# Optimization experiments

Hardware: AMD Instinct MI355X
Metric: run time of the kernel (lower is better)

Reference implementation:

```python
import jax, jax.numpy as jnp
import numpy as np

EPS = 1e-12  # matches tf.math.l2_normalize epsilon used by K.l2_normalize


def setup_inputs() -> dict:
    key = jax.random.key(0)
    k1, k2, k3 = jax.random.split(key, 3)
    B, N, C = 512, 256, 256
    x = jax.random.normal(k1, (B, N, C), dtype=jnp.float32)
    kernel = jax.random.normal(k2, (N, 1), dtype=jnp.float32)
    bias = jax.random.normal(k3, (N,), dtype=jnp.float32)
    return {"x": x, "kernel": kernel, "bias": bias}


def reference(x, kernel, bias):
    # x: [B, N, C]; kernel: [N, 1]; bias: [N]
    N = x.shape[-2]
    mid = N // 2
    # self-similarity: [B, N, N]
    sim = jnp.einsum('bnc,bmc->bnm', x, x)
    # l2-normalize along last axis (tf semantics: x * rsqrt(max(sum(x^2), eps)))
    coe = sim * jax.lax.rsqrt(jnp.maximum(jnp.sum(sim * sim, axis=-1, keepdims=True), EPS))
    # center row scaled by kernel: [B, N, 1]
    coe0 = coe[:, mid, :][..., None] * kernel
    # gating logits: [B, N, 1]
    w = jnp.einsum('bnm,bmk->bnk', coe, coe0) + bias[None, :, None]
    # softmax over spatial axis N, broadcast-multiply with input
    return jax.nn.softmax(w, axis=-2) * x
```

## Files before the change

### kernel.cpp

```cpp
#include <hip/hip_runtime.h>

#define B_N 256
#define B_C 256
#define MID 128
#define NELEM (B_N * B_C)

typedef float f32x4 __attribute__((ext_vector_type(4)));
typedef __bf16 bf16x8 __attribute__((ext_vector_type(8)));
typedef short short8 __attribute__((ext_vector_type(8)));

__device__ __forceinline__ float bf2f(unsigned short h) {
  return __builtin_bit_cast(float, (unsigned int)h << 16);
}

__device__ __forceinline__ short8 cvt8(float4 a, float4 b) {
  union { unsigned short us[8]; short8 v; } P;
  P.us[0] = __builtin_bit_cast(unsigned short, (__bf16)a.x);
  P.us[1] = __builtin_bit_cast(unsigned short, (__bf16)a.y);
  P.us[2] = __builtin_bit_cast(unsigned short, (__bf16)a.z);
  P.us[3] = __builtin_bit_cast(unsigned short, (__bf16)a.w);
  P.us[4] = __builtin_bit_cast(unsigned short, (__bf16)b.x);
  P.us[5] = __builtin_bit_cast(unsigned short, (__bf16)b.y);
  P.us[6] = __builtin_bit_cast(unsigned short, (__bf16)b.z);
  P.us[7] = __builtin_bit_cast(unsigned short, (__bf16)b.w);
  return P.v;
}

__global__ __launch_bounds__(512, 1) void spat_attn(
    const float* __restrict__ x, const float* __restrict__ kern,
    const float* __restrict__ bias, float* __restrict__ out)
{
  __shared__ __align__(16) unsigned short Xs[NELEM];
  __shared__ float smid[B_N];
  __shared__ float r2s[B_N];
  __shared__ float vb[B_N];
  __shared__ float wlog[B_N];
  __shared__ float wexp[B_N];

  const int tid = threadIdx.x;
  const int b = blockIdx.x;
  const float* __restrict__ xb = x + (size_t)b * NELEM;

  const int w  = tid >> 6;
  const int l  = tid & 63;
  const int lr = l & 15;
  const int g  = l >> 4;
  const int sw = lr & 7;
  const int rb0 = 32 * w + lr;
  const int rb1 = rb0 + 16;

  const int sr  = tid >> 1;
  const int sh  = tid & 1;
  const int srs = sr & 7;
  const int sq0 = 4 * sh;
  const float* __restrict__ sbase = xb + sr * B_C + sh * 32;

  f32x4 acc[16][2];
  #pragma unroll
  for (int t = 0; t < 16; ++t) {
    acc[t][0] = {0.f, 0.f, 0.f, 0.f};
    acc[t][1] = {0.f, 0.f, 0.f, 0.f};
  }

  float4 st[8];

  #pragma unroll
  for (int j = 0; j < 8; ++j)
    st[j] = *reinterpret_cast<const float4*>(sbase + 4 * j);
  #pragma unroll
  for (int m = 0; m < 4; ++m)
    *reinterpret_cast<short8*>(&Xs[(sr << 8) + (((sq0 + m) ^ srs) << 3)]) =
        cvt8(st[2 * m], st[2 * m + 1]);
  __syncthreads();

  #pragma unroll
  for (int c = 0; c < 4; ++c) {
    if (c < 3) {
      #pragma unroll
      for (int j = 0; j < 8; ++j)
        st[j] = *reinterpret_cast<const float4*>(sbase + (c + 1) * 64 + 4 * j);
    }
    #pragma unroll
    for (int kk = 2 * c; kk < 2 * c + 2; ++kk) {
      const int qs = (((4 * kk + g) ^ sw) << 3);
      const bf16x8 bf0 = __builtin_bit_cast(bf16x8,
          *reinterpret_cast<const short8*>(&Xs[(rb0 << 8) + qs]));
      const bf16x8 bf1 = __builtin_bit_cast(bf16x8,
          *reinterpret_cast<const short8*>(&Xs[(rb1 << 8) + qs]));
      #pragma unroll
      for (int t = 0; t < 16; ++t) {
        const bf16x8 af = __builtin_bit_cast(bf16x8,
            *reinterpret_cast<const short8*>(&Xs[((16 * t + lr) << 8) + qs]));
        acc[t][0] = __builtin_amdgcn_mfma_f32_16x16x32_bf16(af, bf0, acc[t][0], 0, 0, 0);
        acc[t][1] = __builtin_amdgcn_mfma_f32_16x16x32_bf16(af, bf1, acc[t][1], 0, 0, 0);
      }
    }
    if (c < 3) {
      #pragma unroll
      for (int m = 0; m < 4; ++m)
        *reinterpret_cast<short8*>(
            &Xs[(sr << 8) + (((8 * (c + 1) + sq0 + m) ^ srs) << 3)]) =
            cvt8(st[2 * m], st[2 * m + 1]);
      __syncthreads();
    }
  }

  float rp0 = 0.f, rp1 = 0.f;
  #pragma unroll
  for (int t = 0; t < 16; ++t) {
    #pragma unroll
    for (int r = 0; r < 4; ++r) {
      rp0 += acc[t][0][r] * acc[t][0][r];
      rp1 += acc[t][1][r] * acc[t][1][r];
    }
  }
  rp0 += __shfl_xor(rp0, 16); rp0 += __shfl_xor(rp0, 32);
  rp1 += __shfl_xor(rp1, 16); rp1 += __shfl_xor(rp1, 32);
  if (l < 16) {
    r2s[32 * w + l]      = rp0;
    r2s[32 * w + 16 + l] = rp1;
    smid[32 * w + l]      = acc[8][0][0];
    smid[32 * w + 16 + l] = acc[8][1][0];
  }
  __syncthreads();

  if (tid < B_N) {
    const float rinvm = rsqrtf(fmaxf(r2s[MID], 1e-12f));
    vb[tid] = smid[tid] * rinvm * kern[tid];
  }
  __syncthreads();

  float up0 = 0.f, up1 = 0.f;
  #pragma unroll
  for (int t = 0; t < 16; ++t) {
    #pragma unroll
    for (int r = 0; r < 4; ++r) {
      const float vv = vb[16 * t + 4 * g + r];
      up0 += acc[t][0][r] * vv;
      up1 += acc[t][1][r] * vv;
    }
  }
  up0 += __shfl_xor(up0, 16); up0 += __shfl_xor(up0, 32);
  up1 += __shfl_xor(up1, 16); up1 += __shfl_xor(up1, 32);
  if (l < 16) {
    const int n0 = 32 * w + l, n1 = n0 + 16;
    wlog[n0] = up0 * rsqrtf(fmaxf(r2s[n0], 1e-12f)) + bias[n0];
    wlog[n1] = up1 * rsqrtf(fmaxf(r2s[n1], 1e-12f)) + bias[n1];
  }
  __syncthreads();

  if (tid < 64) {
    const float a0 = wlog[tid], a1 = wlog[tid + 64], a2 = wlog[tid + 128], a3 = wlog[tid + 192];
    float mx = fmaxf(fmaxf(a0, a1), fmaxf(a2, a3));
    #pragma unroll
    for (int off = 32; off >= 1; off >>= 1) mx = fmaxf(mx, __shfl_xor(mx, off));
    const float e0 = __expf(a0 - mx), e1 = __expf(a1 - mx), e2 = __expf(a2 - mx), e3 = __expf(a3 - mx);
    float s = e0 + e1 + e2 + e3;
    #pragma unroll
    for (int off = 32; off >= 1; off >>= 1) s += __shfl_xor(s, off);
    const float inv = 1.0f / s;
    wexp[tid] = e0 * inv; wexp[tid + 64] = e1 * inv;
    wexp[tid + 128] = e2 * inv; wexp[tid + 192] = e3 * inv;
  }
  __syncthreads();

  float* __restrict__ ob = out + (size_t)b * NELEM;
  #pragma unroll 4
  for (int i = 0; i < 16; ++i) {
    const int e8 = i * 4096 + tid * 8;
    const int r = e8 >> 8;
    const int q = (e8 >> 3) & 31;
    union { short8 v; unsigned short us[8]; } P;
    P.v = *reinterpret_cast<const short8*>(&Xs[(r << 8) + ((q ^ (r & 7)) << 3)]);
    const float wt = wexp[r];
    f32x4 o0, o1;
    o0[0] = bf2f(P.us[0]) * wt; o0[1] = bf2f(P.us[1]) * wt;
    o0[2] = bf2f(P.us[2]) * wt; o0[3] = bf2f(P.us[3]) * wt;
    o1[0] = bf2f(P.us[4]) * wt; o1[1] = bf2f(P.us[5]) * wt;
    o1[2] = bf2f(P.us[6]) * wt; o1[3] = bf2f(P.us[7]) * wt;
    *reinterpret_cast<f32x4*>(ob + e8)     = o0;
    *reinterpret_cast<f32x4*>(ob + e8 + 4) = o1;
  }
}

extern "C" void kernel_launch(void* const* d_in, const int* in_sizes, int n_in,
                              void* d_out, int out_size, void* d_ws, size_t ws_size,
                              hipStream_t stream) {
  const float* x    = (const float*)d_in[0];
  const float* kern = (const float*)d_in[1];
  const float* bias = (const float*)d_in[2];
  float* out = (float*)d_out;
  const int nb = in_sizes[0] / NELEM;
  spat_attn<<<dim3(nb), dim3(512), 0, stream>>>(x, kern, bias, out);
}
```

Measured before the change: 70.91 us.

## Stream x through a 64-column LDS chunk to raise occupancy, reread x for output

```diff
diff --git a/kernel.cpp b/kernel.cpp
--- a/kernel.cpp
+++ b/kernel.cpp
@@ -4,14 +4,12 @@
 #define B_C 256
 #define MID 128
 #define NELEM (B_N * B_C)
+#define CK 64
+#define NC 4
 
 typedef float f32x4 __attribute__((ext_vector_type(4)));
 typedef __bf16 bf16x8 __attribute__((ext_vector_type(8)));
 typedef short short8 __attribute__((ext_vector_type(8)));
-
-__device__ __forceinline__ float bf2f(unsigned short h) {
-  return __builtin_bit_cast(float, (unsigned int)h << 16);
-}
 
 __device__ __forceinline__ short8 cvt8(float4 a, float4 b) {
   union { unsigned short us[8]; short8 v; } P;
@@ -26,11 +24,11 @@
   return P.v;
 }
 
-__global__ __launch_bounds__(512, 1) void spat_attn(
+__global__ __launch_bounds__(512, 4) void spat_attn(
     const float* __restrict__ x, const float* __restrict__ kern,
     const float* __restrict__ bias, float* __restrict__ out)
 {
-  __shared__ __align__(16) unsigned short Xs[NELEM];
+  __shared__ __align__(16) unsigned short Xc[B_N * CK];
   __shared__ float smid[B_N];
   __shared__ float r2s[B_N];
   __shared__ float vb[B_N];
@@ -49,12 +47,6 @@
   const int rb0 = 32 * w + lr;
   const int rb1 = rb0 + 16;
 
-  const int sr  = tid >> 1;
-  const int sh  = tid & 1;
-  const int srs = sr & 7;
-  const int sq0 = 4 * sh;
-  const float* __restrict__ sbase = xb + sr * B_C + sh * 32;
-
   f32x4 acc[16][2];
   #pragma unroll
   for (int t = 0; t < 16; ++t) {
@@ -62,46 +54,35 @@
     acc[t][1] = {0.f, 0.f, 0.f, 0.f};
   }
 
-  float4 st[8];
-
-  #pragma unroll
-  for (int j = 0; j < 8; ++j)
-    st[j] = *reinterpret_cast<const float4*>(sbase + 4 * j);
-  #pragma unroll
-  for (int m = 0; m < 4; ++m)
-    *reinterpret_cast<short8*>(&Xs[(sr << 8) + (((sq0 + m) ^ srs) << 3)]) =
-        cvt8(st[2 * m], st[2 * m + 1]);
-  __syncthreads();
-
-  #pragma unroll
-  for (int c = 0; c < 4; ++c) {
-    if (c < 3) {
-      #pragma unroll
-      for (int j = 0; j < 8; ++j)
-        st[j] = *reinterpret_cast<const float4*>(sbase + (c + 1) * 64 + 4 * j);
+  for (int c = 0; c < NC; ++c) {
+    if (c > 0) __syncthreads();
+    #pragma unroll
+    for (int s = 0; s < 4; ++s) {
+      const int e = s * 4096 + tid * 8;
+      const int row = e >> 6;
+      const int col = e & 63;
+      const float* p = xb + row * B_C + c * CK + col;
+      const float4 f0 = *reinterpret_cast<const float4*>(p);
+      const float4 f1 = *reinterpret_cast<const float4*>(p + 4);
+      const int q = col >> 3;
+      *reinterpret_cast<short8*>(&Xc[(row << 6) + ((q ^ (row & 7)) << 3)]) =
+          cvt8(f0, f1);
     }
+    __syncthreads();
     #pragma unroll
-    for (int kk = 2 * c; kk < 2 * c + 2; ++kk) {
-      const int qs = (((4 * kk + g) ^ sw) << 3);
+    for (int kkl = 0; kkl < 2; ++kkl) {
+      const int qs = (((4 * kkl + g) ^ sw) << 3);
       const bf16x8 bf0 = __builtin_bit_cast(bf16x8,
-          *reinterpret_cast<const short8*>(&Xs[(rb0 << 8) + qs]));
+          *reinterpret_cast<const short8*>(&Xc[(rb0 << 6) + qs]));
       const bf16x8 bf1 = __builtin_bit_cast(bf16x8,
-          *reinterpret_cast<const short8*>(&Xs[(rb1 << 8) + qs]));
+          *reinterpret_cast<const short8*>(&Xc[(rb1 << 6) + qs]));
       #pragma unroll
       for (int t = 0; t < 16; ++t) {
         const bf16x8 af = __builtin_bit_cast(bf16x8,
-            *reinterpret_cast<const short8*>(&Xs[((16 * t + lr) << 8) + qs]));
+            *reinterpret_cast<const short8*>(&Xc[((16 * t + lr) << 6) + qs]));
         acc[t][0] = __builtin_amdgcn_mfma_f32_16x16x32_bf16(af, bf0, acc[t][0], 0, 0, 0);
         acc[t][1] = __builtin_amdgcn_mfma_f32_16x16x32_bf16(af, bf1, acc[t][1], 0, 0, 0);
       }
-    }
-    if (c < 3) {
-      #pragma unroll
-      for (int m = 0; m < 4; ++m)
-        *reinterpret_cast<short8*>(
-            &Xs[(sr << 8) + (((8 * (c + 1) + sq0 + m) ^ srs) << 3)]) =
-            cvt8(st[2 * m], st[2 * m + 1]);
-      __syncthreads();
     }
   }
 
@@ -168,16 +149,12 @@
   #pragma unroll 4
   for (int i = 0; i < 16; ++i) {
     const int e8 = i * 4096 + tid * 8;
-    const int r = e8 >> 8;
-    const int q = (e8 >> 3) & 31;
-    union { short8 v; unsigned short us[8]; } P;
-    P.v = *reinterpret_cast<const short8*>(&Xs[(r << 8) + ((q ^ (r & 7)) << 3)]);
-    const float wt = wexp[r];
+    const float wt = wexp[e8 >> 8];
+    const float4 f0 = *reinterpret_cast<const float4*>(xb + e8);
+    const float4 f1 = *reinterpret_cast<const float4*>(xb + e8 + 4);
     f32x4 o0, o1;
-    o0[0] = bf2f(P.us[0]) * wt; o0[1] = bf2f(P.us[1]) * wt;
-    o0[2] = bf2f(P.us[2]) * wt; o0[3] = bf2f(P.us[3]) * wt;
-    o1[0] = bf2f(P.us[4]) * wt; o1[1] = bf2f(P.us[5]) * wt;
-    o1[2] = bf2f(P.us[6]) * wt; o1[3] = bf2f(P.us[7]) * wt;
+    o0[0] = f0.x * wt; o0[1] = f0.y * wt; o0[2] = f0.z * wt; o0[3] = f0.w * wt;
+    o1[0] = f1.x * wt; o1[1] = f1.y * wt; o1[2] = f1.z * wt; o1[3] = f1.w * wt;
     *reinterpret_cast<f32x4*>(ob + e8)     = o0;
     *reinterpret_cast<f32x4*>(ob + e8 + 4) = o1;
   }
```

After: 256.2 us. +261.2%, slower.
